# Kernel tuning notes

Hardware: AMD Instinct MI355X
Metric: run time of the kernel (lower is better)

The kernel has to match this reference:

```python
import jax, jax.numpy as jnp
import numpy as np

B, N, C, H = 8, 1024, 1024, 16
D = C // H
DFF = 4 * C
EPS = 1e-6


def _ln(x):
    mu = jnp.mean(x, axis=-1, keepdims=True)
    var = jnp.mean(jnp.square(x - mu), axis=-1, keepdims=True)
    return (x - mu) / jnp.sqrt(var + EPS)


def _modulate(x, shift, scale):
    return x * (1 + scale) + shift


def setup_inputs() -> dict:
    key = jax.random.key(0)
    ks = jax.random.split(key, 12)
    s = 0.02
    inp = {
        "x": jax.random.normal(ks[0], (B, N, C), jnp.float32),
        "c": jax.random.normal(ks[1], (B, 1, C), jnp.float32),
        "causal_mask": jnp.tril(jnp.ones((N, N), jnp.int32))[None, None],  # [1,1,N,N]
        "qkv_w": jax.random.normal(ks[2], (3 * C, C), jnp.float32) * s,
        "qkv_b": jnp.zeros((3 * C,), jnp.float32),
        "proj_w": jax.random.normal(ks[3], (C, C), jnp.float32) * s,
        "proj_b": jnp.zeros((C,), jnp.float32),
        "fc1_w": jax.random.normal(ks[4], (DFF, C), jnp.float32) * s,
        "fc1_b": jnp.zeros((DFF,), jnp.float32),
        "fc2_w": jax.random.normal(ks[5], (C, DFF), jnp.float32) * s,
        "fc2_b": jnp.zeros((C,), jnp.float32),
        "ada_w": jax.random.normal(ks[6], (6 * C, C), jnp.float32) * s,
        "ada_b": jnp.zeros((6 * C,), jnp.float32),
    }
    return inp


def reference(x, c, causal_mask, qkv_w, qkv_b, proj_w, proj_b,
              fc1_w, fc1_b, fc2_w, fc2_b, ada_w, ada_b):
    # adaLN modulation: SiLU -> Linear(C -> 6C) -> chunk 6
    mod = jax.nn.silu(c) @ ada_w.T + ada_b  # [B,1,6C]
    (shift_msa, scale_msa, gate_msa,
     shift_mlp, scale_mlp, gate_mlp) = jnp.split(mod, 6, axis=-1)

    # --- causal attention ---
    y = _modulate(_ln(x), shift_msa, scale_msa)  # [B,N,C]
    qkv = y @ qkv_w.T + qkv_b                    # [B,N,3C]
    qkv = qkv.reshape(B, N, 3, H, D).transpose(2, 0, 3, 1, 4)  # [3,B,H,N,D]
    q, k, v = qkv[0], qkv[1], qkv[2]
    scale = D ** -0.5
    attn = jnp.einsum('bhnd,bhmd->bhnm', q, k) * scale  # [B,H,N,N]
    attn = jnp.where(causal_mask == 0, -jnp.inf, attn)
    attn = jax.nn.softmax(attn, axis=-1)
    o = jnp.einsum('bhnm,bhmd->bhnd', attn, v)
    o = o.transpose(0, 2, 1, 3).reshape(B, N, C)
    o = o @ proj_w.T + proj_b
    x = x + gate_msa * o

    # --- MLP ---
    z = _modulate(_ln(x), shift_mlp, scale_mlp)
    h = jax.nn.gelu(z @ fc1_w.T + fc1_b, approximate=True)
    m = h @ fc2_w.T + fc2_b
    x = x + gate_mlp * m
    return x
```

## Files before the change

### kernel.cpp

```cpp
#include <hip/hip_runtime.h>
#include <math.h>
#include <stdint.h>
#include <stddef.h>

namespace {

constexpr int kB = 8, kN = 1024, kC = 1024, kH = 16, kD = 64, kDFF = 4096;
constexpr int kM = kB * kN;
constexpr int k6C = 6 * kC;
constexpr float kQKScale = 0.18033688011112042f;
constexpr float kM8 = 8.0f;

typedef _Float16 half8 __attribute__((ext_vector_type(8)));
typedef _Float16 half4v __attribute__((ext_vector_type(4)));
typedef float f32x4 __attribute__((ext_vector_type(4)));
typedef int v4i __attribute__((ext_vector_type(4)));
typedef signed char i8;

__device__ inline void ld_lds16(const void* g, void* l) {
  __builtin_amdgcn_global_load_lds(
      (const __attribute__((address_space(1))) void*)g,
      (__attribute__((address_space(3))) void*)l, 16, 0, 0);
}

__device__ inline unsigned pack4_i8(float y0, float y1, float y2, float y3, float inv) {
  int q0 = (int)rintf(y0 * inv), q1 = (int)rintf(y1 * inv);
  int q2 = (int)rintf(y2 * inv), q3 = (int)rintf(y3 * inv);
  q0 = min(max(q0, -127), 127); q1 = min(max(q1, -127), 127);
  q2 = min(max(q2, -127), 127); q3 = min(max(q3, -127), 127);
  return (unsigned)(q0 & 0xFF) | ((unsigned)(q1 & 0xFF) << 8) |
         ((unsigned)(q2 & 0xFF) << 16) | ((unsigned)(q3 & 0xFF) << 24);
}

__global__ void cvt_f32_f16(const float* __restrict__ src, _Float16* __restrict__ dst) {
  size_t i = (size_t)blockIdx.x * 256 + threadIdx.x;
  float4 f = ((const float4*)src)[i];
  half4v h;
  h[0] = (_Float16)f.x; h[1] = (_Float16)f.y; h[2] = (_Float16)f.z; h[3] = (_Float16)f.w;
  ((half4v*)dst)[i] = h;
}

__global__ __launch_bounds__(256) void quant_w_kernel(
    const float* __restrict__ src, i8* __restrict__ dst, float* __restrict__ wscale) {
  int n = blockIdx.x, tid = threadIdx.x;
  const float* row = src + (size_t)n * kC;
  float4 f = ((const float4*)row)[tid];
  float m = fmaxf(fmaxf(fabsf(f.x), fabsf(f.y)), fmaxf(fabsf(f.z), fabsf(f.w)));
#pragma unroll
  for (int msk = 32; msk; msk >>= 1) m = fmaxf(m, __shfl_xor(m, msk));
  __shared__ float red[4];
  int w = tid >> 6, lane = tid & 63;
  if (lane == 0) red[w] = m;
  __syncthreads();
  m = fmaxf(fmaxf(red[0], red[1]), fmaxf(red[2], red[3]));
  m = fmaxf(m, 1e-12f);
  float inv = 127.f / m;
  ((unsigned*)(dst + (size_t)n * kC))[tid] = pack4_i8(f.x, f.y, f.z, f.w, inv);
  if (tid == 0) wscale[n] = m * (1.f / 127.f);
}

__global__ __launch_bounds__(256) void mod_kernel(
    const float* __restrict__ c, const float* __restrict__ ada_w,
    const float* __restrict__ ada_b, float* __restrict__ mod) {
  __shared__ float sc[kC];
  int b  = blockIdx.x / (k6C / 4);
  int j0 = (blockIdx.x % (k6C / 4)) * 4;
  int tid = threadIdx.x;
  for (int i = tid; i < kC; i += 256) {
    float v = c[b * kC + i];
    sc[i] = v / (1.f + expf(-v));
  }
  __syncthreads();
  int w = tid >> 6, lane = tid & 63;
  int j = j0 + w;
  const float* wr = ada_w + (size_t)j * kC;
  float acc = 0.f;
#pragma unroll
  for (int kk = 0; kk < kC / 64; ++kk) {
    int k = kk * 64 + lane;
    acc += sc[k] * wr[k];
  }
#pragma unroll
  for (int m = 32; m; m >>= 1) acc += __shfl_xor(acc, m);
  if (lane == 0) mod[b * k6C + j] = acc + ada_b[j];
}

template <typename T>
__global__ __launch_bounds__(256) void ln_mod_q_kernel(
    const T* __restrict__ x, const float* __restrict__ mod,
    i8* __restrict__ out, float* __restrict__ ascale,
    int shift_off, int scale_off) {
  int row = blockIdx.x;
  int b = row >> 10;
  const T* xr = x + (size_t)row * kC;
  int tid = threadIdx.x;
  int cc0 = tid * 4;
  float v[4];
  float s = 0.f, s2 = 0.f;
#pragma unroll
  for (int i = 0; i < 4; ++i) {
    v[i] = (float)xr[cc0 + i];
    s += v[i];
    s2 += v[i] * v[i];
  }
#pragma unroll
  for (int m = 32; m; m >>= 1) { s += __shfl_xor(s, m); s2 += __shfl_xor(s2, m); }
  __shared__ float red[8];
  __shared__ float redm[4];
  int w = tid >> 6, lane = tid & 63;
  if (lane == 0) { red[w] = s; red[4 + w] = s2; }
  __syncthreads();
  s  = red[0] + red[1] + red[2] + red[3];
  s2 = red[4] + red[5] + red[6] + red[7];
  float mu   = s * (1.f / kC);
  float var  = s2 * (1.f / kC) - mu * mu;
  float rstd = rsqrtf(var + 1e-6f);
  const float* mb = mod + (size_t)b * k6C;
  float y[4];
  float m = 0.f;
#pragma unroll
  for (int i = 0; i < 4; ++i) {
    y[i] = (v[i] - mu) * rstd * (1.f + mb[scale_off + cc0 + i]) + mb[shift_off + cc0 + i];
    m = fmaxf(m, fabsf(y[i]));
  }
#pragma unroll
  for (int msk = 32; msk; msk >>= 1) m = fmaxf(m, __shfl_xor(m, msk));
  if (lane == 0) redm[w] = m;
  __syncthreads();
  m = fmaxf(fmaxf(redm[0], redm[1]), fmaxf(redm[2], redm[3]));
  m = fmaxf(m, 1e-12f);
  float inv = 127.f / m;
  ((unsigned*)(out + (size_t)row * kC))[tid] = pack4_i8(y[0], y[1], y[2], y[3], inv);
  if (tid == 0) ascale[row] = m * (1.f / 127.f);
}

template <int EPI>
__global__ __launch_bounds__(256) void gemm_i8_kernel(
    const i8* __restrict__ A, const i8* __restrict__ W,
    const float* __restrict__ ascale, const float* __restrict__ wscale,
    const float* __restrict__ bias, _Float16* __restrict__ outp,
    int M, int Nn, int K) {
  __shared__ __align__(16) i8 S[2 * 128 * 128];
  i8* As = S;
  i8* Bs = S + 128 * 128;
  int tid = threadIdx.x;
  int bm = blockIdx.y, bn = blockIdx.x;
  int lane = tid & 63, w = tid >> 6;
  int l15 = lane & 15, quad = lane >> 4;
  int wr = (w >> 1) * 64, wc = (w & 1) * 64;

  v4i acc[4][4];
#pragma unroll
  for (int i = 0; i < 4; ++i)
#pragma unroll
    for (int j = 0; j < 4; ++j) acc[i][j] = (v4i){0, 0, 0, 0};

  const i8* Ag = A + (size_t)bm * 128 * K;
  const i8* Wg = W + (size_t)bn * 128 * K;
  int r8 = lane >> 3;
  int jcb = ((lane & 7) ^ r8) * 16;

  for (int kt = 0; kt < K; kt += 128) {
#pragma unroll
    for (int u = 0; u < 4; ++u) {
      int row = w * 32 + u * 8 + r8;
      ld_lds16(&Ag[(size_t)row * K + kt + jcb], &As[(w * 32 + u * 8) * 128]);
      ld_lds16(&Wg[(size_t)row * K + kt + jcb], &Bs[(w * 32 + u * 8) * 128]);
    }
    __syncthreads();
    int sxor = l15 & 7;
    int c0 = (quad ^ sxor) * 16;
    int c1 = ((4 + quad) ^ sxor) * 16;
    v4i af[4][2], bf[4][2];
#pragma unroll
    for (int i = 0; i < 4; ++i) {
      const i8* rp = &As[(wr + i * 16 + l15) * 128];
      af[i][0] = *(const v4i*)&rp[c0];
      af[i][1] = *(const v4i*)&rp[c1];
    }
#pragma unroll
    for (int j = 0; j < 4; ++j) {
      const i8* rp = &Bs[(wc + j * 16 + l15) * 128];
      bf[j][0] = *(const v4i*)&rp[c0];
      bf[j][1] = *(const v4i*)&rp[c1];
    }
#pragma unroll
    for (int i = 0; i < 4; ++i)
#pragma unroll
      for (int j = 0; j < 4; ++j) {
        acc[i][j] = __builtin_amdgcn_mfma_i32_16x16x64_i8(af[i][0], bf[j][0], acc[i][j], 0, 0, 0);
        acc[i][j] = __builtin_amdgcn_mfma_i32_16x16x64_i8(af[i][1], bf[j][1], acc[i][j], 0, 0, 0);
      }
    __syncthreads();
  }

  _Float16* Cs = (_Float16*)S;
  int row0 = wr + quad * 4;
  int col0 = wc + l15;
#pragma unroll
  for (int i = 0; i < 4; ++i) {
#pragma unroll
    for (int j = 0; j < 4; ++j) {
      int colL = col0 + j * 16;
      int n = bn * 128 + colL;
      float ws = wscale[n];
      float bv = bias[n];
#pragma unroll
      for (int r = 0; r < 4; ++r) {
        int rowL = row0 + i * 16 + r;
        float as = ascale[bm * 128 + rowL];
        float v = (float)acc[i][j][r] * (as * ws) + bv;
        if constexpr (EPI == 0) {
          if (n < kC) v *= kQKScale;
        } else {
          float u = v + 0.044715f * v * v * v;
          v = v / (1.f + exp2f(-2.302208f * u));
        }
        Cs[rowL * 128 + (((colL >> 3) ^ (rowL & 7)) << 3) + (colL & 7)] = (_Float16)v;
      }
    }
  }
  __syncthreads();
#pragma unroll
  for (int p = 0; p < 8; ++p) {
    int r = (tid >> 4) + p * 16;
    int cc = tid & 15;
    half8 hv = *(const half8*)&Cs[r * 128 + ((cc ^ (r & 7)) << 3)];
    size_t gm = (size_t)(bm * 128 + r);
    int coff = bn * 128 + cc * 8;
    *(half8*)&outp[gm * Nn + coff] = hv;
  }
}

template <int EPI>
__global__ __launch_bounds__(256) void gemm_f16_kernel(
    const _Float16* __restrict__ A, const _Float16* __restrict__ W,
    const float* __restrict__ bias, void* __restrict__ outp,
    const void* __restrict__ resid, const float* __restrict__ mod,
    int M, int Nn, int K, int gate_off) {
  __shared__ __align__(16) _Float16 S[128 * 64 * 2];
  _Float16* As = S;
  _Float16* Bs = S + 128 * 64;
  int tid = threadIdx.x;
  int bm = blockIdx.y, bn = blockIdx.x;
  int lane = tid & 63, w = tid >> 6;
  int l15 = lane & 15, quad = lane >> 4;
  int wr = (w >> 1) * 64, wc = (w & 1) * 64;

  f32x4 acc[4][4];
#pragma unroll
  for (int i = 0; i < 4; ++i)
#pragma unroll
    for (int j = 0; j < 4; ++j) acc[i][j] = (f32x4){0.f, 0.f, 0.f, 0.f};

  const _Float16* Ag = A + (size_t)bm * 128 * K;
  const _Float16* Wg = W + (size_t)bn * 128 * K;
  int r8 = lane >> 3;
  int jc = ((lane & 7) ^ r8) * 8;

  for (int kt = 0; kt < K; kt += 64) {
#pragma unroll
    for (int u = 0; u < 4; ++u) {
      int row = w * 32 + u * 8 + r8;
      ld_lds16(&Ag[(size_t)row * K + kt + jc], &As[(w * 32 + u * 8) * 64]);
      ld_lds16(&Wg[(size_t)row * K + kt + jc], &Bs[(w * 32 + u * 8) * 64]);
    }
    __syncthreads();
#pragma unroll
    for (int kk = 0; kk < 2; ++kk) {
      half8 af[4], bf[4];
#pragma unroll
      for (int i = 0; i < 4; ++i)
        af[i] = *(const half8*)&As[(wr + i * 16 + l15) * 64 +
                                   (((kk * 4 + quad) ^ (l15 & 7)) * 8)];
#pragma unroll
      for (int j = 0; j < 4; ++j)
        bf[j] = *(const half8*)&Bs[(wc + j * 16 + l15) * 64 +
                                   (((kk * 4 + quad) ^ (l15 & 7)) * 8)];
#pragma unroll
      for (int i = 0; i < 4; ++i)
#pragma unroll
        for (int j = 0; j < 4; ++j)
          acc[i][j] = __builtin_amdgcn_mfma_f32_16x16x32_f16(af[i], bf[j], acc[i][j], 0, 0, 0);
    }
    __syncthreads();
  }

  _Float16* Cs = S;
  int row0 = wr + quad * 4;
  int col0 = wc + l15;
#pragma unroll
  for (int i = 0; i < 4; ++i) {
#pragma unroll
    for (int j = 0; j < 4; ++j) {
      int colL = col0 + j * 16;
      int n = bn * 128 + colL;
      float bv = bias[n];
#pragma unroll
      for (int r = 0; r < 4; ++r) {
        int rowL = row0 + i * 16 + r;
        float v = acc[i][j][r] + bv;
        Cs[rowL * 128 + (((colL >> 3) ^ (rowL & 7)) << 3) + (colL & 7)] = (_Float16)v;
      }
    }
  }
  __syncthreads();
  int b6 = (bm >> 3) * k6C + gate_off + bn * 128;
#pragma unroll
  for (int p = 0; p < 8; ++p) {
    int r = (tid >> 4) + p * 16;
    int cc = tid & 15;
    half8 hv = *(const half8*)&Cs[r * 128 + ((cc ^ (r & 7)) << 3)];
    size_t gm = (size_t)(bm * 128 + r);
    int coff = bn * 128 + cc * 8;
    if constexpr (EPI == 2) {
      const float* rp = &((const float*)resid)[gm * kC + coff];
      const float* gp = &mod[b6 + cc * 8];
      half8 ov;
#pragma unroll
      for (int e = 0; e < 8; ++e) ov[e] = (_Float16)(rp[e] + gp[e] * (float)hv[e]);
      *(half8*)&((_Float16*)outp)[gm * kC + coff] = ov;
    } else {
      const _Float16* rp = &((const _Float16*)resid)[gm * kC + coff];
      const float* gp = &mod[b6 + cc * 8];
      half8 rv = *(const half8*)rp;
      float ov[8];
#pragma unroll
      for (int e = 0; e < 8; ++e) ov[e] = (float)rv[e] + gp[e] * (float)hv[e];
      *(float4*)&((float*)outp)[gm * kC + coff] = *(float4*)&ov[0];
      *(float4*)&((float*)outp)[gm * kC + coff + 4] = *(float4*)&ov[4];
    }
  }
}

__global__ __launch_bounds__(256) void vtrans_kernel(
    const _Float16* __restrict__ qkv, _Float16* __restrict__ vT) {
  int nt = blockIdx.x, h = blockIdx.y, b = blockIdx.z;
  __shared__ _Float16 Ts[64 * 72];
  int tid = threadIdx.x;
  const _Float16* src = qkv + ((size_t)(b * kN + nt * 64)) * (3 * kC) + 2 * kC + h * 64;
#pragma unroll
  for (int u = 0; u < 2; ++u) {
    int idx = tid + u * 256;
    int r = idx >> 3, c8 = (idx & 7) * 8;
    *(uint4*)&Ts[r * 72 + c8] = *(const uint4*)&src[(size_t)r * (3 * kC) + c8];
  }
  __syncthreads();
  _Float16* dst = vT + (((size_t)(b * kH + h)) * 64) * kN + nt * 64;
#pragma unroll
  for (int u = 0; u < 2; ++u) {
    int idx = tid + u * 256;
    int d = idx >> 3, n8 = (idx & 7) * 8;
    half8 v;
#pragma unroll
    for (int e = 0; e < 8; ++e) v[e] = Ts[(n8 + e) * 72 + d];
    *(half8*)&dst[(size_t)d * kN + n8] = v;
  }
}

__global__ __launch_bounds__(256) void attn_kernel(
    const _Float16* __restrict__ qkv, const _Float16* __restrict__ vT,
    _Float16* __restrict__ o) {
  int qt = blockIdx.x, h = blockIdx.y, b = blockIdx.z;
  __shared__ __align__(16) _Float16 Qs[128 * 64];
  __shared__ __align__(16) _Float16 Ks[64 * 64];
  __shared__ __align__(16) _Float16 Vs[64 * 64];
  __shared__ __align__(16) _Float16 Ps[128 * 72];
  int tid = threadIdx.x, lane = tid & 63, w = tid >> 6;
  int l15 = lane & 15, quad = lane >> 4;
  int wq = w * 32;
  int r8 = lane >> 3;
  int jc = ((lane & 7) ^ r8) * 8;

  const _Float16* Qg = qkv + ((size_t)(b * kN + qt * 128)) * (3 * kC) + h * kD;
  const _Float16* Kg = qkv + ((size_t)(b * kN)) * (3 * kC) + kC + h * kD;
  const _Float16* Vg = vT + ((size_t)(b * kH + h) * kD) * kN;

#pragma unroll
  for (int u = 0; u < 4; ++u)
    ld_lds16(&Qg[(size_t)(w * 32 + u * 8 + r8) * (3 * kC) + jc],
             &Qs[(w * 32 + u * 8) * 64]);
  __syncthreads();

  half8 aq[2][2];
#pragma unroll
  for (int i = 0; i < 2; ++i)
#pragma unroll
    for (int kk = 0; kk < 2; ++kk)
      aq[i][kk] = *(const half8*)&Qs[(wq + i * 16 + l15) * 64 +
                                     (((kk * 4 + quad) ^ (l15 & 7)) * 8)];

  f32x4 o_acc[2][4];
  f32x4 lsum[2];
#pragma unroll
  for (int i = 0; i < 2; ++i) {
    lsum[i] = (f32x4){0.f, 0.f, 0.f, 0.f};
#pragma unroll
    for (int dt = 0; dt < 4; ++dt) o_acc[i][dt] = (f32x4){0.f, 0.f, 0.f, 0.f};
  }
  half8 ones;
#pragma unroll
  for (int e = 0; e < 8; ++e) ones[e] = (_Float16)1.f;

  int jmax = 2 * qt + 2;
  for (int j = 0; j < jmax; ++j) {
#pragma unroll
    for (int u = 0; u < 2; ++u) {
      int row = w * 16 + u * 8 + r8;
      ld_lds16(&Kg[(size_t)(j * 64 + row) * (3 * kC) + jc], &Ks[(w * 16 + u * 8) * 64]);
      ld_lds16(&Vg[(size_t)row * kN + j * 64 + jc],         &Vs[(w * 16 + u * 8) * 64]);
    }
    __syncthreads();
    bool need_mask = (j >= 2 * qt);

    f32x4 s[2][4];
#pragma unroll
    for (int ct = 0; ct < 4; ++ct) {
      half8 b0 = *(const half8*)&Ks[(ct * 16 + l15) * 64 + ((quad ^ (l15 & 7)) * 8)];
      half8 b1 = *(const half8*)&Ks[(ct * 16 + l15) * 64 + (((4 + quad) ^ (l15 & 7)) * 8)];
#pragma unroll
      for (int i = 0; i < 2; ++i) {
        f32x4 t = (f32x4){0.f, 0.f, 0.f, 0.f};
        t = __builtin_amdgcn_mfma_f32_16x16x32_f16(aq[i][0], b0, t, 0, 0, 0);
        t = __builtin_amdgcn_mfma_f32_16x16x32_f16(aq[i][1], b1, t, 0, 0, 0);
        s[i][ct] = t;
      }
    }

#pragma unroll
    for (int i = 0; i < 2; ++i)
#pragma unroll
      for (int ct = 0; ct < 4; ++ct)
#pragma unroll
        for (int r = 0; r < 4; ++r) {
          float p = exp2f(fminf(s[i][ct][r] - kM8, 14.f));
          if (need_mask) {
            int kg = j * 64 + ct * 16 + l15;
            int qg = qt * 128 + wq + i * 16 + quad * 4 + r;
            if (kg > qg) p = 0.f;
          }
          Ps[(wq + i * 16 + quad * 4 + r) * 72 + ct * 16 + l15] = (_Float16)p;
        }

    half8 ap[2][2];
#pragma unroll
    for (int i = 0; i < 2; ++i) {
      ap[i][0] = *(const half8*)&Ps[(wq + i * 16 + l15) * 72 + quad * 8];
      ap[i][1] = *(const half8*)&Ps[(wq + i * 16 + l15) * 72 + 32 + quad * 8];
      lsum[i] = __builtin_amdgcn_mfma_f32_16x16x32_f16(ap[i][0], ones, lsum[i], 0, 0, 0);
      lsum[i] = __builtin_amdgcn_mfma_f32_16x16x32_f16(ap[i][1], ones, lsum[i], 0, 0, 0);
    }
#pragma unroll
    for (int dt = 0; dt < 4; ++dt) {
      half8 bv0 = *(const half8*)&Vs[(dt * 16 + l15) * 64 + ((quad ^ (l15 & 7)) * 8)];
      half8 bv1 = *(const half8*)&Vs[(dt * 16 + l15) * 64 + (((4 + quad) ^ (l15 & 7)) * 8)];
#pragma unroll
      for (int i = 0; i < 2; ++i) {
        o_acc[i][dt] = __builtin_amdgcn_mfma_f32_16x16x32_f16(ap[i][0], bv0, o_acc[i][dt], 0, 0, 0);
        o_acc[i][dt] = __builtin_amdgcn_mfma_f32_16x16x32_f16(ap[i][1], bv1, o_acc[i][dt], 0, 0, 0);
      }
    }
    __syncthreads();
  }

#pragma unroll
  for (int i = 0; i < 2; ++i) {
    float rl[4];
#pragma unroll
    for (int r = 0; r < 4; ++r) rl[r] = 1.f / lsum[i][r];
#pragma unroll
    for (int dt = 0; dt < 4; ++dt)
#pragma unroll
      for (int r = 0; r < 4; ++r) {
        int q = qt * 128 + wq + i * 16 + quad * 4 + r;
        o[((size_t)(b * kN + q)) * kC + h * kD + dt * 16 + l15] =
            (_Float16)(o_acc[i][dt][r] * rl[r]);
      }
  }
}

}

extern "C" void kernel_launch(void* const* d_in, const int* in_sizes, int n_in,
                              void* d_out, int out_size, void* d_ws, size_t ws_size,
                              hipStream_t stream) {
  const float* x      = (const float*)d_in[0];
  const float* c      = (const float*)d_in[1];
  const float* qkv_w  = (const float*)d_in[3];
  const float* qkv_b  = (const float*)d_in[4];
  const float* proj_w = (const float*)d_in[5];
  const float* proj_b = (const float*)d_in[6];
  const float* fc1_w  = (const float*)d_in[7];
  const float* fc1_b  = (const float*)d_in[8];
  const float* fc2_w  = (const float*)d_in[9];
  const float* fc2_b  = (const float*)d_in[10];
  const float* ada_w  = (const float*)d_in[11];
  const float* ada_b  = (const float*)d_in[12];
  float* out = (float*)d_out;

  char* ws = (char*)d_ws;
  float*    mod     = (float*)(ws);
  i8*       w_qkv   = (i8*)(ws + 196608);
  i8*       w_fc1   = (i8*)(ws + 3342336);
  _Float16* w_proj  = (_Float16*)(ws + 7536640);
  _Float16* w_fc2   = (_Float16*)(ws + 9633792);
  i8*       bufA    = (i8*)(ws + 18022400);
  float*    ascale  = (float*)(ws + 26411008);
  float*    ws_qkv  = (float*)(ws + 26443776);
  float*    ws_fc1  = (float*)(ws + 26456064);
  _Float16* vT      = (_Float16*)(ws + 26509312);
  _Float16* x2h     = (_Float16*)(ws + 26509312);
  _Float16* bufO    = (_Float16*)(ws + 43286528);
  _Float16* qkvh    = (_Float16*)(ws + 60063744);
  _Float16* hbuf    = (_Float16*)(ws + 60063744);

  quant_w_kernel<<<3 * kC, 256, 0, stream>>>(qkv_w, w_qkv, ws_qkv);
  quant_w_kernel<<<kDFF, 256, 0, stream>>>(fc1_w, w_fc1, ws_fc1);
  cvt_f32_f16<<<kC * kC / 1024, 256, 0, stream>>>(proj_w, w_proj);
  cvt_f32_f16<<<kC * kDFF / 1024, 256, 0, stream>>>(fc2_w, w_fc2);
  mod_kernel<<<kB * (k6C / 4), 256, 0, stream>>>(c, ada_w, ada_b, mod);
  ln_mod_q_kernel<float><<<kM, 256, 0, stream>>>(x, mod, bufA, ascale, 0, kC);
  gemm_i8_kernel<0><<<dim3(3 * kC / 128, kM / 128), 256, 0, stream>>>(
      bufA, w_qkv, ascale, ws_qkv, qkv_b, qkvh, kM, 3 * kC, kC);
  vtrans_kernel<<<dim3(kN / 64, kH, kB), 256, 0, stream>>>(qkvh, vT);
  attn_kernel<<<dim3(kN / 128, kH, kB), 256, 0, stream>>>(qkvh, vT, bufO);
  gemm_f16_kernel<2><<<dim3(kC / 128, kM / 128), 256, 0, stream>>>(
      bufO, w_proj, proj_b, x2h, x, mod, kM, kC, kC, 2 * kC);
  ln_mod_q_kernel<_Float16><<<kM, 256, 0, stream>>>(x2h, mod, bufA, ascale, 3 * kC, 4 * kC);
  gemm_i8_kernel<1><<<dim3(kDFF / 128, kM / 128), 256, 0, stream>>>(
      bufA, w_fc1, ascale, ws_fc1, fc1_b, hbuf, kM, kDFF, kC);
  gemm_f16_kernel<3><<<dim3(kC / 128, kM / 128), 256, 0, stream>>>(
      hbuf, w_fc2, fc2_b, out, x2h, mod, kM, kC, kDFF, 5 * kC);
}
```

Baseline: 531.4 us.

## Double-buffer f16 GEMM LDS tiles and add XCD-aware block swizzling

```diff
diff --git a/kernel.cpp b/kernel.cpp
--- a/kernel.cpp
+++ b/kernel.cpp
@@ -21,6 +21,10 @@
   __builtin_amdgcn_global_load_lds(
       (const __attribute__((address_space(1))) void*)g,
       (__attribute__((address_space(3))) void*)l, 16, 0, 0);
+}
+
+__device__ inline int xcd_swizzle(int flat, int nwg) {
+  return (flat & 7) * (nwg >> 3) + (flat >> 3);
 }
 
 __device__ inline unsigned pack4_i8(float y0, float y1, float y2, float y3, float inv) {
@@ -144,7 +148,9 @@
   i8* As = S;
   i8* Bs = S + 128 * 128;
   int tid = threadIdx.x;
-  int bm = blockIdx.y, bn = blockIdx.x;
+  int nwg = (int)(gridDim.x * gridDim.y);
+  int swz = xcd_swizzle((int)(blockIdx.y * gridDim.x + blockIdx.x), nwg);
+  int bn = swz % (int)gridDim.x, bm = swz / (int)gridDim.x;
   int lane = tid & 63, w = tid >> 6;
   int l15 = lane & 15, quad = lane >> 4;
   int wr = (w >> 1) * 64, wc = (w & 1) * 64;
@@ -238,11 +244,11 @@
     const float* __restrict__ bias, void* __restrict__ outp,
     const void* __restrict__ resid, const float* __restrict__ mod,
     int M, int Nn, int K, int gate_off) {
-  __shared__ __align__(16) _Float16 S[128 * 64 * 2];
-  _Float16* As = S;
-  _Float16* Bs = S + 128 * 64;
+  __shared__ __align__(16) _Float16 S[2 * 2 * 128 * 64];
   int tid = threadIdx.x;
-  int bm = blockIdx.y, bn = blockIdx.x;
+  int nwg = (int)(gridDim.x * gridDim.y);
+  int swz = xcd_swizzle((int)(blockIdx.y * gridDim.x + blockIdx.x), nwg);
+  int bn = swz % (int)gridDim.x, bm = swz / (int)gridDim.x;
   int lane = tid & 63, w = tid >> 6;
   int l15 = lane & 15, quad = lane >> 4;
   int wr = (w >> 1) * 64, wc = (w & 1) * 64;
@@ -258,14 +264,33 @@
   int r8 = lane >> 3;
   int jc = ((lane & 7) ^ r8) * 8;
 
-  for (int kt = 0; kt < K; kt += 64) {
+  int nk = K / 64;
+  {
+    _Float16* Asp = S;
+    _Float16* Bsp = S + 128 * 64;
 #pragma unroll
     for (int u = 0; u < 4; ++u) {
       int row = w * 32 + u * 8 + r8;
-      ld_lds16(&Ag[(size_t)row * K + kt + jc], &As[(w * 32 + u * 8) * 64]);
-      ld_lds16(&Wg[(size_t)row * K + kt + jc], &Bs[(w * 32 + u * 8) * 64]);
-    }
-    __syncthreads();
+      ld_lds16(&Ag[(size_t)row * K + jc], &Asp[(w * 32 + u * 8) * 64]);
+      ld_lds16(&Wg[(size_t)row * K + jc], &Bsp[(w * 32 + u * 8) * 64]);
+    }
+  }
+  __syncthreads();
+
+  for (int t = 0; t < nk; ++t) {
+    const _Float16* As = S + (t & 1) * (2 * 128 * 64);
+    const _Float16* Bs = As + 128 * 64;
+    if (t + 1 < nk) {
+      _Float16* Asn = S + ((t + 1) & 1) * (2 * 128 * 64);
+      _Float16* Bsn = Asn + 128 * 64;
+      int kt = (t + 1) * 64;
+#pragma unroll
+      for (int u = 0; u < 4; ++u) {
+        int row = w * 32 + u * 8 + r8;
+        ld_lds16(&Ag[(size_t)row * K + kt + jc], &Asn[(w * 32 + u * 8) * 64]);
+        ld_lds16(&Wg[(size_t)row * K + kt + jc], &Bsn[(w * 32 + u * 8) * 64]);
+      }
+    }
 #pragma unroll
     for (int kk = 0; kk < 2; ++kk) {
       half8 af[4], bf[4];
@@ -361,7 +386,12 @@
 __global__ __launch_bounds__(256) void attn_kernel(
     const _Float16* __restrict__ qkv, const _Float16* __restrict__ vT,
     _Float16* __restrict__ o) {
-  int qt = blockIdx.x, h = blockIdx.y, b = blockIdx.z;
+  int nwg = (int)(gridDim.x * gridDim.y * gridDim.z);
+  int flat = (int)((blockIdx.z * gridDim.y + blockIdx.y) * gridDim.x + blockIdx.x);
+  int swz = xcd_swizzle(flat, nwg);
+  int qt = swz % (int)gridDim.x;
+  int tmp = swz / (int)gridDim.x;
+  int h = tmp % (int)gridDim.y, b = tmp / (int)gridDim.y;
   __shared__ __align__(16) _Float16 Qs[128 * 64];
   __shared__ __align__(16) _Float16 Ks[64 * 64];
   __shared__ __align__(16) _Float16 Vs[64 * 64];
```

New measurement: 478.1 us. 1.11x faster.
